# Optimization experiments

Hardware: AMD Instinct MI355X
Metric: run time of the kernel (lower is better)

The kernel has to match this reference:

```python
import jax, jax.numpy as jnp
import numpy as np

N = 50000    # nodes
E = 800000   # edges (avg degree 16)
F = 256      # input feats_dim
H = 4        # num_heads
D = 64       # out_feats per head
HD = H * D   # 256


def setup_inputs() -> dict:
    key = jax.random.key(0)
    ks = jax.random.split(key, 16)
    s = 0.05
    inp = {
        "feat": jax.random.normal(ks[0], (N, F), jnp.float32),
        "src": jax.random.randint(ks[1], (E,), 0, N, dtype=jnp.int32),
        "dst": jax.random.randint(ks[2], (E,), 0, N, dtype=jnp.int32),
        "Wq": jax.random.normal(ks[3], (F, HD), jnp.float32) * s,
        "bq": jnp.zeros((HD,), jnp.float32),
        "Wk": jax.random.normal(ks[4], (F, HD), jnp.float32) * s,
        "bk": jnp.zeros((HD,), jnp.float32),
        "Wv": jax.random.normal(ks[5], (F, HD), jnp.float32) * s,
        "bv": jnp.zeros((HD,), jnp.float32),
        "Wskip": jax.random.normal(ks[6], (F, HD), jnp.float32) * s,
        "bskip": jnp.zeros((HD,), jnp.float32),
        "Wg": jax.random.normal(ks[7], (3 * HD, 1), jnp.float32) * s,
        "bg": jnp.zeros((1,), jnp.float32),
        "ln_scale": jnp.ones((HD,), jnp.float32),
        "ln_bias": jnp.zeros((HD,), jnp.float32),
        "prelu_alpha": jnp.asarray(0.25, jnp.float32),
    }
    return inp


def reference(feat, src, dst, Wq, bq, Wk, bk, Wv, bv, Wskip, bskip,
              Wg, bg, ln_scale, ln_bias, prelu_alpha):
    n = feat.shape[0]
    # QKV projections -> [N, H, D]
    q = (feat @ Wq + bq).reshape(n, H, D)   # lives on src nodes (DGL 'ft' srcdata)
    k = (feat @ Wk + bk).reshape(n, H, D)   # lives on dst nodes (DGL 'ft' dstdata)
    v = (feat @ Wv + bv).reshape(n, H, D)

    # Per-edge per-head score: u_dot_v(q, k) / sqrt(D)   -> [E, H]
    score = jnp.einsum('ehd,ehd->eh', q[src], k[dst]) / np.sqrt(D).astype(np.float32)

    # edge_softmax over incoming edges of each destination node (numerically stable)
    m = jax.ops.segment_max(score, dst, num_segments=n)        # [N, H]
    a = jnp.exp(score - m[dst])                                # [E, H]
    denom = jax.ops.segment_sum(a, dst, num_segments=n)       # [N, H]
    sa = a / denom[dst]                                        # [E, H]

    # u_mul_e + sum aggregation at dst -> [N, H, D] -> [N, H*D]
    agg = jax.ops.segment_sum(v[src] * sa[..., None], dst, num_segments=n)
    rst = agg.reshape(n, HD)

    # gated skip connection
    skip = feat @ Wskip + bskip                                # [N, HD]
    gate = jax.nn.sigmoid(
        jnp.concatenate([skip, rst, skip - rst], axis=-1) @ Wg + bg)  # [N, 1]
    rst = gate * skip + (1.0 - gate) * rst

    # LayerNorm over feature dim
    mu = rst.mean(axis=-1, keepdims=True)
    var = rst.var(axis=-1, keepdims=True)
    rst = (rst - mu) * jax.lax.rsqrt(var + 1e-5) * ln_scale + ln_bias

    # PReLU (single shared alpha, torch default init 0.25)
    return jnp.where(rst > 0, rst, prelu_alpha * rst)
```

## Files before the change

kernel.cpp:

```cpp
#include <hip/hip_runtime.h>
#include <hip/hip_bf16.h>

typedef __attribute__((ext_vector_type(4))) float f32x4;
typedef __attribute__((ext_vector_type(8))) short bf16x8;
typedef __attribute__((ext_vector_type(8))) unsigned short us8;
typedef __attribute__((ext_vector_type(4))) unsigned short us4;

#define MAXDEG 64

__device__ __forceinline__ float bf2f(unsigned short u) {
    union { unsigned int i; float f; } x; x.i = ((unsigned int)u) << 16; return x.f;
}
__device__ __forceinline__ unsigned short f2bf(float f) {
    union { float f; unsigned int i; } x; x.f = f;
    unsigned int i = x.i;
    return (unsigned short)((i + 0x7FFFu + ((i >> 16) & 1u)) >> 16);
}

__global__ void k_conv_w(const float* __restrict__ Wq, const float* __restrict__ Wk,
                         const float* __restrict__ Wv, const float* __restrict__ Ws,
                         const float* __restrict__ bq, const float* __restrict__ bk,
                         const float* __restrict__ bv, const float* __restrict__ bs,
                         const float* __restrict__ Wg,
                         unsigned short* __restrict__ Wt, float* __restrict__ ball,
                         float* __restrict__ wga, float* __restrict__ wgb)
{
    int gid = blockIdx.x * 256 + threadIdx.x;
    int k = gid >> 8, colq = gid & 255;
    int col0 = colq * 4;
    const float* Wsel[4] = {Wq, Wk, Wv, Ws};
    const float* W = Wsel[col0 >> 8];
    int c0 = col0 & 255;
    f32x4 w = *(const f32x4*)(W + k * 256 + c0);
    for (int j = 0; j < 4; ++j)
        Wt[(size_t)(col0 + j) * 256 + k] = f2bf(w[j]);
    if (gid < 1024) {
        const float* bsel[4] = {bq, bk, bv, bs};
        ball[gid] = bsel[gid >> 8][gid & 255];
    } else if (gid < 1280) {
        int i = gid - 1024;
        wga[i] = Wg[i] + Wg[512 + i];
    } else if (gid < 1536) {
        int i = gid - 1280;
        wgb[i] = Wg[256 + i] - Wg[512 + i];
    }
}

#define BM 64
#define BN 128
#define BK 64
#define SST 72

__global__ __launch_bounds__(256, 4) void k_gemm(
    const float* __restrict__ A, const unsigned short* __restrict__ Bt,
    const float* __restrict__ bias, unsigned short* __restrict__ qkvb2,
    const int* __restrict__ src, const int* __restrict__ dst,
    int* __restrict__ cnt, int* __restrict__ esrcF,
    int M, int MB, int EB, int E)
{
    __shared__ unsigned short a_sm[BM * SST];
    __shared__ unsigned short b_sm[BN * SST];
    int id = blockIdx.x;
    int k3 = id / 3;
    if ((id % 3) == 2 && k3 < EB) {
        int t2 = k3 * 256 + threadIdx.x;
        if (t2 < E) {
            int d = dst[t2];
            int slot = atomicAdd(&cnt[d], 1);
            if (slot < MAXDEG) esrcF[(size_t)d * MAXDEG + slot] = src[t2];
        }
        return;
    }
    int slots_before = (id + 1) / 3;
    if (slots_before > EB) slots_before = EB;
    int gid = id - slots_before;
    int rr = gid & 7, bn = (gid >> 3) & 7, bm = (gid >> 6) * 8 + rr;
    if (bm >= MB) return;
    int t = threadIdx.x;
    int lane = t & 63, wid = t >> 6;
    int wc = wid;
    int l15 = lane & 15, l4 = lane >> 4;

    int asrow[2], asko[2];
    const float* pa[2];
    for (int it = 0; it < 2; ++it) {
        int c = it * 256 + t;
        int row = c >> 3, ko = (c & 7) * 8;
        asrow[it] = row; asko[it] = ko;
        int grow = bm * BM + row;
        if (grow >= M) grow = M - 1;
        pa[it] = A + (size_t)grow * 256 + ko;
    }
    int bsrow[4], bsko[4];
    const unsigned short* pb[4];
    for (int it = 0; it < 4; ++it) {
        int c = it * 256 + t;
        int row = c >> 3, ko = (c & 7) * 8;
        bsrow[it] = row; bsko[it] = ko;
        pb[it] = Bt + (size_t)(bn * BN + row) * 256 + ko;
    }

    f32x4 rax[2], ray[2];
    us8 rvb[4];
    auto load_ab = [&](int k0) {
        #pragma unroll
        for (int it = 0; it < 2; ++it) {
            const f32x4* p = (const f32x4*)(pa[it] + k0);
            rax[it] = p[0]; ray[it] = p[1];
        }
        #pragma unroll
        for (int it = 0; it < 4; ++it)
            rvb[it] = *(const us8*)(pb[it] + k0);
    };

    f32x4 acc[4][2] = {};
    load_ab(0);
    for (int k0 = 0; k0 < 256; k0 += BK) {
        #pragma unroll
        for (int it = 0; it < 2; ++it) {
            us8 o;
            o[0] = f2bf(rax[it][0]); o[1] = f2bf(rax[it][1]);
            o[2] = f2bf(rax[it][2]); o[3] = f2bf(rax[it][3]);
            o[4] = f2bf(ray[it][0]); o[5] = f2bf(ray[it][1]);
            o[6] = f2bf(ray[it][2]); o[7] = f2bf(ray[it][3]);
            *(us8*)(a_sm + asrow[it] * SST + asko[it]) = o;
        }
        #pragma unroll
        for (int it = 0; it < 4; ++it)
            *(us8*)(b_sm + bsrow[it] * SST + bsko[it]) = rvb[it];
        __syncthreads();
        if (k0 + BK < 256) load_ab(k0 + BK);
        for (int kk = 0; kk < BK; kk += 32) {
            bf16x8 af[4], bf[2];
            for (int mi = 0; mi < 4; ++mi)
                af[mi] = *(const bf16x8*)(a_sm + (mi * 16 + l15) * SST + kk + l4 * 8);
            for (int ni = 0; ni < 2; ++ni)
                bf[ni] = *(const bf16x8*)(b_sm + (wc * 32 + ni * 16 + l15) * SST + kk + l4 * 8);
            for (int mi = 0; mi < 4; ++mi)
                for (int ni = 0; ni < 2; ++ni)
                    acc[mi][ni] = __builtin_amdgcn_mfma_f32_16x16x32_bf16(af[mi], bf[ni], acc[mi][ni], 0, 0, 0);
        }
        __syncthreads();
    }
    int colb = bn * BN + wc * 32 + l15;
    for (int mi = 0; mi < 4; ++mi) {
        int rowb = bm * BM + mi * 16 + l4 * 4;
        for (int ni = 0; ni < 2; ++ni) {
            int col = colb + ni * 16;
            float bv = bias[col];
            int ocol = (col < 256) ? col : (col < 512) ? col + 256 : (col < 768) ? col - 256 : col;
            for (int r = 0; r < 4; ++r) {
                int row = rowb + r;
                if (row < M) {
                    float v = acc[mi][ni][r] + bv;
                    qkvb2[(size_t)row * 1024 + ocol] = f2bf(v);
                }
            }
        }
    }
}

__device__ __forceinline__ float dot4k(us4 q, const float* kf) {
    return bf2f(q[0]) * kf[0] + bf2f(q[1]) * kf[1] + bf2f(q[2]) * kf[2] + bf2f(q[3]) * kf[3];
}
__device__ __forceinline__ float red16(float sc) {
    sc += __shfl_xor(sc, 1, 16);
    sc += __shfl_xor(sc, 2, 16);
    sc += __shfl_xor(sc, 4, 16);
    sc += __shfl_xor(sc, 8, 16);
    return sc;
}

__global__ void k_attn(const unsigned short* __restrict__ qkvb2,
                       const int* __restrict__ cnt, const int* __restrict__ esrcF,
                       const float* __restrict__ wga, const float* __restrict__ wgb,
                       const float* __restrict__ bgp, const float* __restrict__ lns,
                       const float* __restrict__ lnb, const float* __restrict__ alphap,
                       float* __restrict__ out, int n)
{
    int node = blockIdx.x * 4 + (threadIdx.x >> 6);
    if (node >= n) return;
    int lane = threadIdx.x & 63;
    int lane4 = lane * 4;
    const unsigned short* nrow = qkvb2 + (size_t)node * 1024;
    us4 k4 = __builtin_nontemporal_load((const us4*)(nrow + 512 + lane4));
    float kf[4];
    for (int i = 0; i < 4; ++i) kf[i] = bf2f(k4[i]);
    int deg = cnt[node];
    if (deg > MAXDEG) deg = MAXDEG;
    const int* ep = esrcF + (size_t)node * MAXDEG;
    float denom = 0.f;
    f32x4 acc = {0.f, 0.f, 0.f, 0.f};
    int p = 0;
    for (; p + 8 <= deg; p += 8) {
        int sidx[8];
        #pragma unroll
        for (int j = 0; j < 8; ++j) sidx[j] = ep[p + j];
        us4 q[8], v[8];
        #pragma unroll
        for (int j = 0; j < 8; ++j) {
            const unsigned short* r = qkvb2 + (size_t)sidx[j] * 1024 + lane4;
            q[j] = *(const us4*)(r);
            v[j] = *(const us4*)(r + 256);
        }
        float a[8];
        #pragma unroll
        for (int j = 0; j < 8; ++j)
            a[j] = __expf(red16(dot4k(q[j], kf)) * 0.125f);
        #pragma unroll
        for (int j = 0; j < 8; ++j) {
            denom += a[j];
            for (int i = 0; i < 4; ++i) acc[i] += a[j] * bf2f(v[j][i]);
        }
    }
    for (; p + 4 <= deg; p += 4) {
        int sidx[4];
        #pragma unroll
        for (int j = 0; j < 4; ++j) sidx[j] = ep[p + j];
        us4 q[4], v[4];
        #pragma unroll
        for (int j = 0; j < 4; ++j) {
            const unsigned short* r = qkvb2 + (size_t)sidx[j] * 1024 + lane4;
            q[j] = *(const us4*)(r);
            v[j] = *(const us4*)(r + 256);
        }
        float a[4];
        #pragma unroll
        for (int j = 0; j < 4; ++j)
            a[j] = __expf(red16(dot4k(q[j], kf)) * 0.125f);
        #pragma unroll
        for (int j = 0; j < 4; ++j) {
            denom += a[j];
            for (int i = 0; i < 4; ++i) acc[i] += a[j] * bf2f(v[j][i]);
        }
    }
    for (; p < deg; ++p) {
        int s = ep[p];
        const unsigned short* r = qkvb2 + (size_t)s * 1024 + lane4;
        us4 q4 = *(const us4*)(r);
        us4 v4 = *(const us4*)(r + 256);
        float sc = red16(dot4k(q4, kf));
        float a = __expf(sc * 0.125f);
        denom += a;
        for (int i = 0; i < 4; ++i) acc[i] += a * bf2f(v4[i]);
    }
    float inv = denom > 0.f ? 1.f / denom : 0.f;
    float rst[4];
    for (int i = 0; i < 4; ++i) rst[i] = acc[i] * inv;

    us4 sk4 = __builtin_nontemporal_load((const us4*)(nrow + 768 + lane4));
    float sk[4];
    for (int i = 0; i < 4; ++i) sk[i] = bf2f(sk4[i]);
    f32x4 ga = *(const f32x4*)(wga + lane4);
    f32x4 gb = *(const f32x4*)(wgb + lane4);
    float g = 0.f;
    for (int i = 0; i < 4; ++i) g += sk[i] * ga[i] + rst[i] * gb[i];
    for (int off = 1; off < 64; off <<= 1) g += __shfl_xor(g, off, 64);
    float gate = 1.f / (1.f + __expf(-(g + bgp[0])));
    float r[4], s1v = 0.f, s2v = 0.f;
    for (int i = 0; i < 4; ++i) {
        r[i] = gate * sk[i] + (1.f - gate) * rst[i];
        s1v += r[i]; s2v += r[i] * r[i];
    }
    for (int off = 1; off < 64; off <<= 1) {
        s1v += __shfl_xor(s1v, off, 64);
        s2v += __shfl_xor(s2v, off, 64);
    }
    float mean = s1v * (1.f / 256.f);
    float var = s2v * (1.f / 256.f) - mean * mean;
    float rsig = rsqrtf(var + 1e-5f);
    f32x4 sc4 = *(const f32x4*)(lns + lane4);
    f32x4 bi4 = *(const f32x4*)(lnb + lane4);
    float alpha = alphap[0];
    f32x4 y;
    for (int i = 0; i < 4; ++i) {
        float v = (r[i] - mean) * rsig * sc4[i] + bi4[i];
        y[i] = v > 0.f ? v : alpha * v;
    }
    __builtin_nontemporal_store(y, (f32x4*)(out + (size_t)node * 256 + lane4));
}

extern "C" void kernel_launch(void* const* d_in, const int* in_sizes, int n_in,
                              void* d_out, int out_size, void* d_ws, size_t ws_size,
                              hipStream_t stream)
{
    const float* feat = (const float*)d_in[0];
    const int* src = (const int*)d_in[1];
    const int* dst = (const int*)d_in[2];
    const float* Wq = (const float*)d_in[3];
    const float* bq = (const float*)d_in[4];
    const float* Wk = (const float*)d_in[5];
    const float* bk = (const float*)d_in[6];
    const float* Wv = (const float*)d_in[7];
    const float* bv = (const float*)d_in[8];
    const float* Ws = (const float*)d_in[9];
    const float* bs = (const float*)d_in[10];
    const float* Wg = (const float*)d_in[11];
    const float* bg = (const float*)d_in[12];
    const float* lns = (const float*)d_in[13];
    const float* lnb = (const float*)d_in[14];
    const float* alpha = (const float*)d_in[15];
    int N = in_sizes[0] / 256;
    int E = in_sizes[1];

    char* w = (char*)d_ws;
    size_t off = 0;
    auto alloc = [&](size_t b) { char* p = w + off; off += (b + 255) & ~(size_t)255; return p; };
    unsigned short* Wt    = (unsigned short*)alloc((size_t)1024 * 256 * 2);
    float* ball = (float*)alloc(1024 * 4);
    float* wga  = (float*)alloc(256 * 4);
    float* wgb  = (float*)alloc(256 * 4);
    unsigned short* qkvb2 = (unsigned short*)alloc((size_t)N * 1024 * 2);
    int* cnt = (int*)alloc((size_t)N * 4);
    int* esrcF = (int*)alloc((size_t)N * MAXDEG * 4);
    float* outf = (float*)d_out;

    hipMemsetAsync(cnt, 0, (size_t)N * 4, stream);

    k_conv_w<<<256, 256, 0, stream>>>(Wq, Wk, Wv, Ws, bq, bk, bv, bs, Wg, Wt, ball, wga, wgb);

    int MB = (N + BM - 1) / BM;
    int GB = ((MB + 7) / 8) * 64;
    int eb = (E + 255) / 256;
    k_gemm<<<GB + eb, 256, 0, stream>>>(feat, Wt, ball, qkvb2,
                                        src, dst, cnt, esrcF, N, MB, eb, E);

    k_attn<<<(N + 3) / 4, 256, 0, stream>>>(qkvb2, cnt, esrcF,
                                            wga, wgb, bg, lns, lnb, alpha, outf, N);
}
```

Baseline: 211.2 us.

## Load GEMM operands directly from global memory into MFMA fragments, dropping LDS staging

The QKV/skip GEMM no longer stages A and B tiles through shared memory with __syncthreads. Each wave now loads its own A rows (converting fp32 to bf16 in registers) and B columns straight from global memory into MFMA operand fragments, fully unrolled over K. This removes the LDS writes and reads and the barriers. In exchange, every one of the four waves reloads and reconverts the same A tile, so redundant global/L2 traffic and conversion work go up, and accesses are strided per lane.

```diff
diff --git a/kernel.cpp b/kernel.cpp
--- a/kernel.cpp
+++ b/kernel.cpp
@@ -48,8 +48,6 @@
 
 #define BM 64
 #define BN 128
-#define BK 64
-#define SST 72
 
 __global__ __launch_bounds__(256, 4) void k_gemm(
     const float* __restrict__ A, const unsigned short* __restrict__ Bt,
@@ -58,8 +56,6 @@
     int* __restrict__ cnt, int* __restrict__ esrcF,
     int M, int MB, int EB, int E)
 {
-    __shared__ unsigned short a_sm[BM * SST];
-    __shared__ unsigned short b_sm[BN * SST];
     int id = blockIdx.x;
     int k3 = id / 3;
     if ((id % 3) == 2 && k3 < EB) {
@@ -77,70 +73,48 @@
     int rr = gid & 7, bn = (gid >> 3) & 7, bm = (gid >> 6) * 8 + rr;
     if (bm >= MB) return;
     int t = threadIdx.x;
-    int lane = t & 63, wid = t >> 6;
-    int wc = wid;
+    int lane = t & 63, wc = t >> 6;
     int l15 = lane & 15, l4 = lane >> 4;
 
-    int asrow[2], asko[2];
-    const float* pa[2];
-    for (int it = 0; it < 2; ++it) {
-        int c = it * 256 + t;
-        int row = c >> 3, ko = (c & 7) * 8;
-        asrow[it] = row; asko[it] = ko;
-        int grow = bm * BM + row;
-        if (grow >= M) grow = M - 1;
-        pa[it] = A + (size_t)grow * 256 + ko;
-    }
-    int bsrow[4], bsko[4];
-    const unsigned short* pb[4];
-    for (int it = 0; it < 4; ++it) {
-        int c = it * 256 + t;
-        int row = c >> 3, ko = (c & 7) * 8;
-        bsrow[it] = row; bsko[it] = ko;
-        pb[it] = Bt + (size_t)(bn * BN + row) * 256 + ko;
-    }
-
-    f32x4 rax[2], ray[2];
-    us8 rvb[4];
-    auto load_ab = [&](int k0) {
-        #pragma unroll
-        for (int it = 0; it < 2; ++it) {
-            const f32x4* p = (const f32x4*)(pa[it] + k0);
-            rax[it] = p[0]; ray[it] = p[1];
-        }
-        #pragma unroll
-        for (int it = 0; it < 4; ++it)
-            rvb[it] = *(const us8*)(pb[it] + k0);
-    };
+    const float* pa[4];
+    #pragma unroll
+    for (int mi = 0; mi < 4; ++mi) {
+        int row = bm * BM + mi * 16 + l15;
+        if (row >= M) row = M - 1;
+        pa[mi] = A + (size_t)row * 256 + l4 * 8;
+    }
+    const unsigned short* pb[2];
+    #pragma unroll
+    for (int ni = 0; ni < 2; ++ni) {
+        int col = bn * BN + wc * 32 + ni * 16 + l15;
+        pb[ni] = Bt + (size_t)col * 256 + l4 * 8;
+    }
 
     f32x4 acc[4][2] = {};
-    load_ab(0);
-    for (int k0 = 0; k0 < 256; k0 += BK) {
-        #pragma unroll
-        for (int it = 0; it < 2; ++it) {
-            us8 o;
-            o[0] = f2bf(rax[it][0]); o[1] = f2bf(rax[it][1]);
-            o[2] = f2bf(rax[it][2]); o[3] = f2bf(rax[it][3]);
-            o[4] = f2bf(ray[it][0]); o[5] = f2bf(ray[it][1]);
-            o[6] = f2bf(ray[it][2]); o[7] = f2bf(ray[it][3]);
-            *(us8*)(a_sm + asrow[it] * SST + asko[it]) = o;
-        }
-        #pragma unroll
-        for (int it = 0; it < 4; ++it)
-            *(us8*)(b_sm + bsrow[it] * SST + bsko[it]) = rvb[it];
-        __syncthreads();
-        if (k0 + BK < 256) load_ab(k0 + BK);
-        for (int kk = 0; kk < BK; kk += 32) {
-            bf16x8 af[4], bf[2];
-            for (int mi = 0; mi < 4; ++mi)
-                af[mi] = *(const bf16x8*)(a_sm + (mi * 16 + l15) * SST + kk + l4 * 8);
+    #pragma unroll
+    for (int ks = 0; ks < 8; ++ks) {
+        int ko = ks * 32;
+        bf16x8 af[4];
+        #pragma unroll
+        for (int mi = 0; mi < 4; ++mi) {
+            const f32x4* p = (const f32x4*)(pa[mi] + ko);
+            f32x4 x = p[0], y = p[1];
+            union { us8 u; bf16x8 b; } cv;
+            cv.u[0] = f2bf(x[0]); cv.u[1] = f2bf(x[1]);
+            cv.u[2] = f2bf(x[2]); cv.u[3] = f2bf(x[3]);
+            cv.u[4] = f2bf(y[0]); cv.u[5] = f2bf(y[1]);
+            cv.u[6] = f2bf(y[2]); cv.u[7] = f2bf(y[3]);
+            af[mi] = cv.b;
+        }
+        bf16x8 bf[2];
+        #pragma unroll
+        for (int ni = 0; ni < 2; ++ni)
+            bf[ni] = *(const bf16x8*)(pb[ni] + ko);
+        #pragma unroll
+        for (int mi = 0; mi < 4; ++mi)
+            #pragma unroll
             for (int ni = 0; ni < 2; ++ni)
-                bf[ni] = *(const bf16x8*)(b_sm + (wc * 32 + ni * 16 + l15) * SST + kk + l4 * 8);
-            for (int mi = 0; mi < 4; ++mi)
-                for (int ni = 0; ni < 2; ++ni)
-                    acc[mi][ni] = __builtin_amdgcn_mfma_f32_16x16x32_bf16(af[mi], bf[ni], acc[mi][ni], 0, 0, 0);
-        }
-        __syncthreads();
+                acc[mi][ni] = __builtin_amdgcn_mfma_f32_16x16x32_bf16(af[mi], bf[ni], acc[mi][ni], 0, 0, 0);
     }
     int colb = bn * BN + wc * 32 + l15;
     for (int mi = 0; mi < 4; ++mi) {
```

After: 376.2 us. +78.1%, slower.
